# Performance work log

Hardware: AMD Instinct MI355X
Metric: run time of the kernel (lower is better)

The kernel has to match this reference:

```python
import jax, jax.numpy as jnp
import numpy as np

B, I, H, S = 16384, 256, 256, 32
EVENT_THRESH = 0.85


def setup_inputs() -> dict:
    key = jax.random.key(0)
    ks = jax.random.split(key, 20)
    r = lambda k, shp: jax.random.normal(k, shp, dtype=jnp.float32)
    w = lambda k, shp: jax.random.normal(k, shp, dtype=jnp.float32) * 0.02
    return {
        # forward args / state
        "x_t": r(ks[0], (B, I)),
        "h_lstm": r(ks[1], (B, H)),
        "c_lstm": r(ks[2], (B, H)),
        "h_mem_prev": jnp.zeros((B, H), jnp.float32),
        "slots": r(ks[3], (B, S, I)),
        "ptr": jax.random.randint(ks[4], (B,), 0, S, dtype=jnp.int64),
        # SequenceMemoryCell params (weights stored as (in, out))
        "W_val": w(ks[5], (I, I)),
        "b_val": jnp.zeros((I,), jnp.float32),
        "W_ev": w(ks[6], (I, 1)),
        "b_ev": jnp.zeros((1,), jnp.float32),
        "pos_emb": r(ks[7], (S, I)),
        "slot_weights": jnp.ones((S,), jnp.float32),
        "W_sp": w(ks[8], (I, H)),
        "b_sp": jnp.zeros((H,), jnp.float32),
        # LSTM params
        "W_ih": w(ks[9], (I + H, 4 * H)),
        "b_ih": jnp.zeros((4 * H,), jnp.float32),
        "W_hh": w(ks[10], (H, 4 * H)),
    }


def reference(x_t, h_lstm, c_lstm, h_mem_prev, slots, ptr,
              W_val, b_val, W_ev, b_ev, pos_emb, slot_weights, W_sp, b_sp,
              W_ih, b_ih, W_hh):
    n_slots = slot_weights.shape[0]
    # --- SequenceMemoryCell ---
    e_t = jax.nn.sigmoid(x_t @ W_ev + b_ev)            # (B, 1)
    v = x_t @ W_val + b_val                            # (B, I)
    event_mask = e_t[:, 0] > EVENT_THRESH              # (B,)
    # circular-buffer scatter write at ptr, gated by event_mask
    onehot = jnp.arange(n_slots)[None, :] == ptr[:, None]          # (B, S)
    write = event_mask[:, None] & onehot                           # (B, S)
    new_slots = jnp.where(write[:, :, None], v[:, None, :], slots) # (B, S, I)
    new_ptr = (ptr + event_mask.astype(ptr.dtype)) % n_slots
    # weighted pool over slots with positional embeddings
    w = jax.nn.softmax(slot_weights)                               # (S,)
    pooled = jnp.einsum('bsi,s->bi', new_slots + pos_emb[None], w) # (B, I)
    h_mem = pooled @ W_sp + b_sp                                   # (B, H)
    # --- LSTM on [x_t; h_mem] ---
    gates = jnp.concatenate([x_t, h_mem], axis=1) @ W_ih + b_ih + h_lstm @ W_hh
    i_g, f_g, g_t, o_g = jnp.split(gates, 4, axis=1)
    c_new = jax.nn.sigmoid(f_g) * c_lstm + jax.nn.sigmoid(i_g) * jnp.tanh(g_t)
    h_new = jax.nn.sigmoid(o_g) * jnp.tanh(c_new)
    return (h_new, c_new, h_mem, new_slots, new_ptr)
```

## Files before the change

### kernel.cpp

```cpp
#include <hip/hip_runtime.h>
#include <hip/hip_bf16.h>

#define B_SZ 16384
#define I_SZ 256
#define H_SZ 256
#define S_SZ 32

typedef __attribute__((ext_vector_type(8))) short short8;
typedef __attribute__((ext_vector_type(4))) float f32x4;

__device__ __forceinline__ ushort f2b(float f) {
  __hip_bfloat16 h = __float2bfloat16(f);
  return *reinterpret_cast<ushort*>(&h);
}
__device__ __forceinline__ float sgm(float x) { return 1.0f / (1.0f + expf(-x)); }

__device__ __forceinline__ void gll16(const void* g, void* l) {
  __builtin_amdgcn_global_load_lds(
      (const __attribute__((address_space(1))) unsigned*)g,
      (__attribute__((address_space(3))) unsigned*)l, 16, 0, 0);
}

__global__ __launch_bounds__(256) void front(
    const float* __restrict__ x_t, const float* __restrict__ h_lstm,
    const float* __restrict__ slots, const int* __restrict__ ptr,
    const float* __restrict__ W_val, const float* __restrict__ b_val,
    const float* __restrict__ W_ev, const float* __restrict__ b_ev,
    const float* __restrict__ pos_emb, const float* __restrict__ slot_w,
    const float* __restrict__ W_sp, const float* __restrict__ W_ih,
    const float* __restrict__ W_hh, const float* __restrict__ b_ih,
    const float* __restrict__ b_sp,
    float* __restrict__ out_slots, float* __restrict__ out_ptr,
    ushort* __restrict__ x_b, ushort* __restrict__ hl_b,
    ushort* __restrict__ pooled_b, ushort* __restrict__ WspT,
    ushort* __restrict__ WcatT, float* __restrict__ biasp) {
  __shared__ float x_sh[4][256];
  const int bid = blockIdx.x;
  const int t = threadIdx.x;

  if (bid < 4096) {
    int l = t & 63;
    int w = t >> 6;
    int b = bid * 4 + w;

    float4 x4 = *(const float4*)(x_t + (size_t)b * 256 + l * 4);
    *(float4*)&x_sh[w][l * 4] = x4;
    ushort4 xb = make_ushort4(f2b(x4.x), f2b(x4.y), f2b(x4.z), f2b(x4.w));
    *(ushort4*)&x_b[(size_t)b * 256 + l * 4] = xb;
    float4 hl4 = *(const float4*)(h_lstm + (size_t)b * 256 + l * 4);
    ushort4 hb = make_ushort4(f2b(hl4.x), f2b(hl4.y), f2b(hl4.z), f2b(hl4.w));
    *(ushort4*)&hl_b[(size_t)b * 256 + l * 4] = hb;

    float4 we4 = *(const float4*)(W_ev + l * 4);
    float p = x4.x * we4.x + x4.y * we4.y + x4.z * we4.z + x4.w * we4.w;
    for (int off = 32; off; off >>= 1) p += __shfl_xor(p, off, 64);
    float z = p + b_ev[0];
    bool ev = sgm(z) > 0.85f;
    int pb = ptr[b];

    __syncthreads();

    f32x4 v4 = {0.f, 0.f, 0.f, 0.f};
    if (ev) {
      v4 = *(const f32x4*)(b_val + l * 4);
      for (int k = 0; k < 256; k++) {
        float xv = x_sh[w][k];
        f32x4 wv = *(const f32x4*)(W_val + (size_t)k * 256 + l * 4);
        v4 += xv * wv;
      }
    }

    float mx = -1e30f;
    for (int s = 0; s < 32; s++) mx = fmaxf(mx, slot_w[s]);
    float sum = 0.f;
    for (int s = 0; s < 32; s++) sum += expf(slot_w[s] - mx);
    float rs = 1.f / sum;

    const f32x4* sl4 = (const f32x4*)slots + (size_t)b * 2048;
    f32x4* os4 = (f32x4*)out_slots + (size_t)b * 2048;
    const f32x4* pe4 = (const f32x4*)pos_emb;
    f32x4 pool = {0.f, 0.f, 0.f, 0.f};
#pragma unroll 8
    for (int s = 0; s < 32; s++) {
      float ws_ = expf(slot_w[s] - mx) * rs;
      f32x4 tv = __builtin_nontemporal_load(sl4 + s * 64 + l);
      if (ev && s == pb) tv = v4;
      __builtin_nontemporal_store(tv, os4 + s * 64 + l);
      f32x4 pe = pe4[s * 64 + l];
      pool += ws_ * (tv + pe);
    }
    ushort4 pb4 = make_ushort4(f2b(pool[0]), f2b(pool[1]), f2b(pool[2]), f2b(pool[3]));
    *(ushort4*)&pooled_b[(size_t)b * 256 + l * 4] = pb4;

    if (l == 0) out_ptr[b] = (float)(ev ? ((pb + 1) & 31) : pb);

  } else if (bid < 4104) {
    for (int e = (bid - 4096) * 256 + t; e < 65536; e += 8 * 256) {
      int n = e >> 8, k = e & 255;
      WspT[e] = f2b(W_sp[k * 256 + n]);
    }
  } else if (bid < 4168) {
    for (int e = (bid - 4104) * 256 + t; e < 1024 * 512; e += 64 * 256) {
      int r = e >> 9, kk = e & 511;
      int k = (kk < 256) ? kk : kk + 256;
      int hb = r >> 6, g = (r >> 4) & 3, hl = r & 15;
      int n = g * 256 + hb * 16 + hl;
      float v = (k < 512) ? W_ih[(size_t)k * 1024 + n]
                          : W_hh[(size_t)(k - 512) * 1024 + n];
      WcatT[(size_t)r * 768 + k] = f2b(v);
    }
  } else if (bid < 4424) {
    int i = bid - 4168;
    x_sh[0][t] = W_sp[(size_t)i * 256 + t];
    __syncthreads();
    int n0 = t * 4;
    f32x4 acc = {0.f, 0.f, 0.f, 0.f};
    for (int m = 0; m < 256; m++) {
      float s = x_sh[0][m];
      f32x4 w2 = *(const f32x4*)(W_ih + (size_t)(256 + m) * 1024 + n0);
      acc += s * w2;
    }
#pragma unroll
    for (int d = 0; d < 4; d++) {
      int n = n0 + d;
      int g = n >> 8, rem = n & 255, hb = rem >> 4, hl = rem & 15;
      int r = hb * 64 + g * 16 + hl;
      WcatT[(size_t)r * 768 + 256 + i] = f2b(acc[d]);
    }
  } else {
    int n0 = t * 4;
    f32x4 acc = *(const f32x4*)(b_ih + n0);
    for (int m = 0; m < 256; m++) {
      float s = b_sp[m];
      f32x4 w2 = *(const f32x4*)(W_ih + (size_t)(256 + m) * 1024 + n0);
      acc += s * w2;
    }
    *(f32x4*)(biasp + n0) = acc;
  }
}

__global__ __launch_bounds__(256) void gemm_hmem(
    const ushort* __restrict__ A0, const ushort* __restrict__ WT,
    const float* __restrict__ bias, float* __restrict__ out_f32) {
  int l = threadIdx.x & 63;
  int wid = threadIdx.x >> 6;
  int wm = wid >> 1, wn = wid & 1;
  int m0 = blockIdx.x * 128;
  int n0 = blockIdx.y * 128;
  __shared__ ushort Ash[128 * 32];
  __shared__ ushort Bsh[128 * 32];

  f32x4 acc[4][4] = {};

  for (int k0 = 0; k0 < 256; k0 += 32) {
#pragma unroll
    for (int i = 0; i < 2; i++) {
      int seg = i * 256 + threadIdx.x;
      int row = seg >> 2, cb = (seg & 3) * 8;
      gll16(A0 + (size_t)(m0 + row) * 256 + k0 + cb, Ash + seg * 8);
    }
#pragma unroll
    for (int i = 0; i < 2; i++) {
      int seg = i * 256 + threadIdx.x;
      int row = seg >> 2, cb = (seg & 3) * 8;
      gll16(WT + (size_t)(n0 + row) * 256 + k0 + cb, Bsh + seg * 8);
    }
    __syncthreads();

    short8 af[4], bfr[4];
#pragma unroll
    for (int m = 0; m < 4; m++)
      af[m] = *(const short8*)&Ash[(wm * 64 + m * 16 + (l & 15)) * 32 + (l >> 4) * 8];
#pragma unroll
    for (int n = 0; n < 4; n++)
      bfr[n] = *(const short8*)&Bsh[(wn * 64 + n * 16 + (l & 15)) * 32 + (l >> 4) * 8];
#pragma unroll
    for (int m = 0; m < 4; m++)
#pragma unroll
      for (int n = 0; n < 4; n++)
        acc[m][n] = __builtin_amdgcn_mfma_f32_16x16x32_bf16(af[m], bfr[n], acc[m][n], 0, 0, 0);
    __syncthreads();
  }

#pragma unroll
  for (int m = 0; m < 4; m++)
#pragma unroll
    for (int n = 0; n < 4; n++)
#pragma unroll
      for (int r = 0; r < 4; r++) {
        int row = m0 + wm * 64 + m * 16 + (l >> 4) * 4 + r;
        int col = n0 + wn * 64 + n * 16 + (l & 15);
        out_f32[(size_t)row * 256 + col] = acc[m][n][r] + bias[col];
      }
}

template <int KTOT>
__global__ __launch_bounds__(512) void gemm256_lstm(
    const ushort* __restrict__ A0s, const ushort* __restrict__ A1s,
    const ushort* __restrict__ A2s, const ushort* __restrict__ WT,
    const float* __restrict__ bias, const float* __restrict__ c_lstm,
    float* __restrict__ h_out, float* __restrict__ c_out) {
  constexpr int NT = KTOT / 64;
  __shared__ ushort Ash[2][2][128][64];
  __shared__ ushort Bsh[2][2][128][64];
  const int tid = threadIdx.x;
  const int l = tid & 63;
  const int wid = tid >> 6;
  const int wm = wid >> 2, wn = wid & 3;
  const int id = blockIdx.x;
  const int xcd = id & 7, jj = id >> 3;
  const int mb = xcd * 8 + (jj >> 2), nb = jj & 3;
  const int m0 = mb * 256, n0 = nb * 256;

  auto asel = [&](int kt) { return kt < 4 ? A0s : (kt < 8 ? A1s : A2s); };

  auto stageA = [&](int bu, int h, int kt) {
    const ushort* s = asel(kt);
    int cb = (kt & 3) * 64;
#pragma unroll
    for (int ld = 0; ld < 2; ld++) {
      int seg = ld * 512 + tid;
      int row = seg >> 3, C = seg & 7;
      int Cs = C ^ (row & 7);
      gll16(s + (size_t)(m0 + h * 128 + row) * 256 + cb + Cs * 8,
            &Ash[bu][h][0][0] + seg * 8);
    }
  };
  auto stageB = [&](int bu, int h, int kt) {
    int cb = kt * 64;
#pragma unroll
    for (int ld = 0; ld < 2; ld++) {
      int seg = ld * 512 + tid;
      int row = seg >> 3, C = seg & 7;
      int Cs = C ^ (row & 7);
      gll16(WT + (size_t)(n0 + h * 128 + row) * KTOT + cb + Cs * 8,
            &Bsh[bu][h][0][0] + seg * 8);
    }
  };

  f32x4 acc[8][4] = {};

  stageB(0, 0, 0); stageB(0, 1, 0);
  stageA(0, 0, 0); stageA(0, 1, 0);
  stageB(1, 0, 1); stageB(1, 1, 1);

  for (int t = 0; t < NT; t++) {
    const int c = t & 1;
    const ushort* Abase = &Ash[c][wm][0][0];
    const ushort* Bbase = &Bsh[c][wn >> 1][0][0];

    if (t < NT - 1) asm volatile("s_waitcnt vmcnt(4)" ::: "memory");
    else            asm volatile("s_waitcnt vmcnt(0)" ::: "memory");
    asm volatile("s_barrier" ::: "memory");

    short8 bfr[4][2];
#pragma unroll
    for (int nf = 0; nf < 4; nf++)
#pragma unroll
      for (int kk = 0; kk < 2; kk++) {
        int r = (wn & 1) * 64 + nf * 16 + (l & 15);
        int C = (kk * 4 + (l >> 4)) ^ (l & 7);
        bfr[nf][kk] = *(const short8*)(Bbase + r * 64 + C * 8);
      }
    short8 af[2][2];
#pragma unroll
    for (int q = 0; q < 2; q++)
#pragma unroll
      for (int kk = 0; kk < 2; kk++) {
        int r = (0 * 2 + q) * 16 + (l & 15);
        int C = (kk * 4 + (l >> 4)) ^ (l & 7);
        af[q][kk] = *(const short8*)(Abase + r * 64 + C * 8);
      }
    if (t + 1 < NT) stageA(c ^ 1, 0, t + 1);
    __builtin_amdgcn_s_setprio(1);
#pragma unroll
    for (int q = 0; q < 2; q++)
#pragma unroll
      for (int nf = 0; nf < 4; nf++)
#pragma unroll
        for (int kk = 0; kk < 2; kk++)
          acc[q][nf] = __builtin_amdgcn_mfma_f32_16x16x32_bf16(
              af[q][kk], bfr[nf][kk], acc[q][nf], 0, 0, 0);
    __builtin_amdgcn_s_setprio(0);

#pragma unroll
    for (int p = 1; p < 4; p++) {
      asm volatile("s_barrier" ::: "memory");
#pragma unroll
      for (int q = 0; q < 2; q++)
#pragma unroll
        for (int kk = 0; kk < 2; kk++) {
          int r = (p * 2 + q) * 16 + (l & 15);
          int C = (kk * 4 + (l >> 4)) ^ (l & 7);
          af[q][kk] = *(const short8*)(Abase + r * 64 + C * 8);
        }
      if (p == 1) {
        if (t + 1 < NT) stageA(c ^ 1, 1, t + 1);
        if (t + 2 < NT) stageB(c, 0, t + 2);
      } else if (p == 2) {
        if (t + 2 < NT) stageB(c, 1, t + 2);
      }
      __builtin_amdgcn_s_setprio(1);
#pragma unroll
      for (int q = 0; q < 2; q++)
#pragma unroll
        for (int nf = 0; nf < 4; nf++)
#pragma unroll
          for (int kk = 0; kk < 2; kk++)
            acc[p * 2 + q][nf] = __builtin_amdgcn_mfma_f32_16x16x32_bf16(
                af[q][kk], bfr[nf][kk], acc[p * 2 + q][nf], 0, 0, 0);
      __builtin_amdgcn_s_setprio(0);
    }
  }

  int h = (nb * 4 + wn) * 16 + (l & 15);
  float bi = bias[h], bf_ = bias[256 + h], bg = bias[512 + h], bo = bias[768 + h];
#pragma unroll
  for (int mf = 0; mf < 8; mf++)
#pragma unroll
    for (int r = 0; r < 4; r++) {
      int row = m0 + wm * 128 + mf * 16 + (l >> 4) * 4 + r;
      float ig = acc[mf][0][r] + bi;
      float fg = acc[mf][1][r] + bf_;
      float gt = acc[mf][2][r] + bg;
      float og = acc[mf][3][r] + bo;
      float cc = c_lstm[(size_t)row * 256 + h];
      float cn = sgm(fg) * cc + sgm(ig) * tanhf(gt);
      float hn = sgm(og) * tanhf(cn);
      c_out[(size_t)row * 256 + h] = cn;
      h_out[(size_t)row * 256 + h] = hn;
    }
}

extern "C" void kernel_launch(void* const* d_in, const int* in_sizes, int n_in,
                              void* d_out, int out_size, void* d_ws, size_t ws_size,
                              hipStream_t stream) {
  const float* x_t    = (const float*)d_in[0];
  const float* h_lstm = (const float*)d_in[1];
  const float* c_lstm = (const float*)d_in[2];
  const float* slots  = (const float*)d_in[4];
  const int*   ptr    = (const int*)d_in[5];
  const float* W_val  = (const float*)d_in[6];
  const float* b_val  = (const float*)d_in[7];
  const float* W_ev   = (const float*)d_in[8];
  const float* b_ev   = (const float*)d_in[9];
  const float* pos_emb = (const float*)d_in[10];
  const float* slot_w  = (const float*)d_in[11];
  const float* W_sp   = (const float*)d_in[12];
  const float* b_sp   = (const float*)d_in[13];
  const float* W_ih   = (const float*)d_in[14];
  const float* b_ih   = (const float*)d_in[15];
  const float* W_hh   = (const float*)d_in[16];

  float* out = (float*)d_out;
  const size_t BH = (size_t)B_SZ * H_SZ;
  float* out_h    = out;
  float* out_c    = out + BH;
  float* out_hmem = out + 2 * BH;
  float* out_slots = out + 3 * BH;
  float* out_ptr   = out + 3 * BH + (size_t)B_SZ * S_SZ * I_SZ;

  char* ws = (char*)d_ws;
  ushort* x_b      = (ushort*)(ws);
  ushort* hl_b     = (ushort*)(ws + 8388608);
  ushort* pooled_b = (ushort*)(ws + 16777216);
  ushort* WspT     = (ushort*)(ws + 25165824);
  ushort* WcatT    = (ushort*)(ws + 25296896);
  float*  biasp    = (float*)(ws + 26869760);

  front<<<4425, 256, 0, stream>>>(
      x_t, h_lstm, slots, ptr, W_val, b_val, W_ev, b_ev, pos_emb, slot_w,
      W_sp, W_ih, W_hh, b_ih, b_sp,
      out_slots, out_ptr, x_b, hl_b, pooled_b, WspT, WcatT, biasp);

  gemm256_lstm<768><<<256, 512, 0, stream>>>(
      x_b, pooled_b, hl_b, WcatT, biasp, c_lstm, out_h, out_c);

  gemm_hmem<<<dim3(128, 2), 256, 0, stream>>>(
      pooled_b, WspT, b_sp, out_hmem);
}
```

Baseline: 251.4 us.

## Fold h_mem GEMM into LSTM GEMM launch and precompute softmax weights in LDS

Removes the separate gemm_hmem kernel and adds 64 extra blocks to the LSTM GEMM launch. Each of these blocks computes a 256x256 tile of pooled@W_sp with the same pipelined 256-tile loop, using 4 K-steps instead of 12. This saves a launch and its tail, and puts the small h_mem GEMM on CUs left idle by the 256-block main grid. Separately, the front kernel computes the slot softmax once per block with wave shuffles and stores it in shared memory, instead of every thread looping over slot_w with exp. The trade-off is a runtime tile count (nt) and block-type branches inside the GEMM kernel, which may cost some unrolling or register efficiency.

Measured after the change: 253.1 us. No clear change (+0.7%).

```diff
diff --git a/kernel.cpp b/kernel.cpp
--- a/kernel.cpp
+++ b/kernel.cpp
@@ -35,6 +35,7 @@
     ushort* __restrict__ pooled_b, ushort* __restrict__ WspT,
     ushort* __restrict__ WcatT, float* __restrict__ biasp) {
   __shared__ float x_sh[4][256];
+  __shared__ float w_sh[32];
   const int bid = blockIdx.x;
   const int t = threadIdx.x;
 
@@ -42,6 +43,18 @@
     int l = t & 63;
     int w = t >> 6;
     int b = bid * 4 + w;
+
+    if (t < 32) {
+      float v = slot_w[t];
+      float m = v;
+#pragma unroll
+      for (int off = 16; off; off >>= 1) m = fmaxf(m, __shfl_xor(m, off));
+      float e = expf(v - m);
+      float s2 = e;
+#pragma unroll
+      for (int off = 16; off; off >>= 1) s2 += __shfl_xor(s2, off);
+      w_sh[t] = e / s2;
+    }
 
     float4 x4 = *(const float4*)(x_t + (size_t)b * 256 + l * 4);
     *(float4*)&x_sh[w][l * 4] = x4;
@@ -70,19 +83,13 @@
       }
     }
 
-    float mx = -1e30f;
-    for (int s = 0; s < 32; s++) mx = fmaxf(mx, slot_w[s]);
-    float sum = 0.f;
-    for (int s = 0; s < 32; s++) sum += expf(slot_w[s] - mx);
-    float rs = 1.f / sum;
-
     const f32x4* sl4 = (const f32x4*)slots + (size_t)b * 2048;
     f32x4* os4 = (f32x4*)out_slots + (size_t)b * 2048;
     const f32x4* pe4 = (const f32x4*)pos_emb;
     f32x4 pool = {0.f, 0.f, 0.f, 0.f};
 #pragma unroll 8
     for (int s = 0; s < 32; s++) {
-      float ws_ = expf(slot_w[s] - mx) * rs;
+      float ws_ = w_sh[s];
       f32x4 tv = __builtin_nontemporal_load(sl4 + s * 64 + l);
       if (ev && s == pb) tv = v4;
       __builtin_nontemporal_store(tv, os4 + s * 64 + l);
@@ -139,68 +146,14 @@
   }
 }
 
-__global__ __launch_bounds__(256) void gemm_hmem(
-    const ushort* __restrict__ A0, const ushort* __restrict__ WT,
-    const float* __restrict__ bias, float* __restrict__ out_f32) {
-  int l = threadIdx.x & 63;
-  int wid = threadIdx.x >> 6;
-  int wm = wid >> 1, wn = wid & 1;
-  int m0 = blockIdx.x * 128;
-  int n0 = blockIdx.y * 128;
-  __shared__ ushort Ash[128 * 32];
-  __shared__ ushort Bsh[128 * 32];
-
-  f32x4 acc[4][4] = {};
-
-  for (int k0 = 0; k0 < 256; k0 += 32) {
-#pragma unroll
-    for (int i = 0; i < 2; i++) {
-      int seg = i * 256 + threadIdx.x;
-      int row = seg >> 2, cb = (seg & 3) * 8;
-      gll16(A0 + (size_t)(m0 + row) * 256 + k0 + cb, Ash + seg * 8);
-    }
-#pragma unroll
-    for (int i = 0; i < 2; i++) {
-      int seg = i * 256 + threadIdx.x;
-      int row = seg >> 2, cb = (seg & 3) * 8;
-      gll16(WT + (size_t)(n0 + row) * 256 + k0 + cb, Bsh + seg * 8);
-    }
-    __syncthreads();
-
-    short8 af[4], bfr[4];
-#pragma unroll
-    for (int m = 0; m < 4; m++)
-      af[m] = *(const short8*)&Ash[(wm * 64 + m * 16 + (l & 15)) * 32 + (l >> 4) * 8];
-#pragma unroll
-    for (int n = 0; n < 4; n++)
-      bfr[n] = *(const short8*)&Bsh[(wn * 64 + n * 16 + (l & 15)) * 32 + (l >> 4) * 8];
-#pragma unroll
-    for (int m = 0; m < 4; m++)
-#pragma unroll
-      for (int n = 0; n < 4; n++)
-        acc[m][n] = __builtin_amdgcn_mfma_f32_16x16x32_bf16(af[m], bfr[n], acc[m][n], 0, 0, 0);
-    __syncthreads();
-  }
-
-#pragma unroll
-  for (int m = 0; m < 4; m++)
-#pragma unroll
-    for (int n = 0; n < 4; n++)
-#pragma unroll
-      for (int r = 0; r < 4; r++) {
-        int row = m0 + wm * 64 + m * 16 + (l >> 4) * 4 + r;
-        int col = n0 + wn * 64 + n * 16 + (l & 15);
-        out_f32[(size_t)row * 256 + col] = acc[m][n][r] + bias[col];
-      }
-}
-
 template <int KTOT>
-__global__ __launch_bounds__(512) void gemm256_lstm(
+__global__ __launch_bounds__(512) void gemm256_fused(
     const ushort* __restrict__ A0s, const ushort* __restrict__ A1s,
     const ushort* __restrict__ A2s, const ushort* __restrict__ WT,
-    const float* __restrict__ bias, const float* __restrict__ c_lstm,
-    float* __restrict__ h_out, float* __restrict__ c_out) {
-  constexpr int NT = KTOT / 64;
+    const ushort* __restrict__ WspT, const float* __restrict__ bias,
+    const float* __restrict__ b_sp, const float* __restrict__ c_lstm,
+    float* __restrict__ h_out, float* __restrict__ c_out,
+    float* __restrict__ hmem_out) {
   __shared__ ushort Ash[2][2][128][64];
   __shared__ ushort Bsh[2][2][128][64];
   const int tid = threadIdx.x;
@@ -208,11 +161,23 @@
   const int wid = tid >> 6;
   const int wm = wid >> 2, wn = wid & 3;
   const int id = blockIdx.x;
-  const int xcd = id & 7, jj = id >> 3;
-  const int mb = xcd * 8 + (jj >> 2), nb = jj & 3;
-  const int m0 = mb * 256, n0 = nb * 256;
-
-  auto asel = [&](int kt) { return kt < 4 ? A0s : (kt < 8 ? A1s : A2s); };
+  const bool hm = id >= 256;
+  int m0, n0, nb = 0;
+  if (!hm) {
+    const int xcd = id & 7, jj = id >> 3;
+    const int mb = xcd * 8 + (jj >> 2);
+    nb = jj & 3;
+    m0 = mb * 256; n0 = nb * 256;
+  } else {
+    m0 = (id - 256) * 256; n0 = 0;
+  }
+  const int nt = hm ? 4 : 12;
+  const ushort* Bp = hm ? WspT : WT;
+  const int Bstride = hm ? 256 : KTOT;
+
+  auto asel = [&](int kt) {
+    return hm ? A1s : (kt < 4 ? A0s : (kt < 8 ? A1s : A2s));
+  };
 
   auto stageA = [&](int bu, int h, int kt) {
     const ushort* s = asel(kt);
@@ -233,7 +198,7 @@
       int seg = ld * 512 + tid;
       int row = seg >> 3, C = seg & 7;
       int Cs = C ^ (row & 7);
-      gll16(WT + (size_t)(n0 + h * 128 + row) * KTOT + cb + Cs * 8,
+      gll16(Bp + (size_t)(n0 + h * 128 + row) * Bstride + cb + Cs * 8,
             &Bsh[bu][h][0][0] + seg * 8);
     }
   };
@@ -244,12 +209,12 @@
   stageA(0, 0, 0); stageA(0, 1, 0);
   stageB(1, 0, 1); stageB(1, 1, 1);
 
-  for (int t = 0; t < NT; t++) {
+  for (int t = 0; t < nt; t++) {
     const int c = t & 1;
     const ushort* Abase = &Ash[c][wm][0][0];
     const ushort* Bbase = &Bsh[c][wn >> 1][0][0];
 
-    if (t < NT - 1) asm volatile("s_waitcnt vmcnt(4)" ::: "memory");
+    if (t < nt - 1) asm volatile("s_waitcnt vmcnt(4)" ::: "memory");
     else            asm volatile("s_waitcnt vmcnt(0)" ::: "memory");
     asm volatile("s_barrier" ::: "memory");
 
@@ -271,7 +236,7 @@
         int C = (kk * 4 + (l >> 4)) ^ (l & 7);
         af[q][kk] = *(const short8*)(Abase + r * 64 + C * 8);
       }
-    if (t + 1 < NT) stageA(c ^ 1, 0, t + 1);
+    if (t + 1 < nt) stageA(c ^ 1, 0, t + 1);
     __builtin_amdgcn_s_setprio(1);
 #pragma unroll
     for (int q = 0; q < 2; q++)
@@ -295,10 +260,10 @@
           af[q][kk] = *(const short8*)(Abase + r * 64 + C * 8);
         }
       if (p == 1) {
-        if (t + 1 < NT) stageA(c ^ 1, 1, t + 1);
-        if (t + 2 < NT) stageB(c, 0, t + 2);
+        if (t + 1 < nt) stageA(c ^ 1, 1, t + 1);
+        if (t + 2 < nt) stageB(c, 0, t + 2);
       } else if (p == 2) {
-        if (t + 2 < NT) stageB(c, 1, t + 2);
+        if (t + 2 < nt) stageB(c, 1, t + 2);
       }
       __builtin_amdgcn_s_setprio(1);
 #pragma unroll
@@ -313,23 +278,38 @@
     }
   }
 
-  int h = (nb * 4 + wn) * 16 + (l & 15);
-  float bi = bias[h], bf_ = bias[256 + h], bg = bias[512 + h], bo = bias[768 + h];
-#pragma unroll
-  for (int mf = 0; mf < 8; mf++)
-#pragma unroll
-    for (int r = 0; r < 4; r++) {
-      int row = m0 + wm * 128 + mf * 16 + (l >> 4) * 4 + r;
-      float ig = acc[mf][0][r] + bi;
-      float fg = acc[mf][1][r] + bf_;
-      float gt = acc[mf][2][r] + bg;
-      float og = acc[mf][3][r] + bo;
-      float cc = c_lstm[(size_t)row * 256 + h];
-      float cn = sgm(fg) * cc + sgm(ig) * tanhf(gt);
-      float hn = sgm(og) * tanhf(cn);
-      c_out[(size_t)row * 256 + h] = cn;
-      h_out[(size_t)row * 256 + h] = hn;
-    }
+  if (!hm) {
+    int h = (nb * 4 + wn) * 16 + (l & 15);
+    float bi = bias[h], bf_ = bias[256 + h], bg = bias[512 + h], bo = bias[768 + h];
+#pragma unroll
+    for (int mf = 0; mf < 8; mf++)
+#pragma unroll
+      for (int r = 0; r < 4; r++) {
+        int row = m0 + wm * 128 + mf * 16 + (l >> 4) * 4 + r;
+        float ig = acc[mf][0][r] + bi;
+        float fg = acc[mf][1][r] + bf_;
+        float gt = acc[mf][2][r] + bg;
+        float og = acc[mf][3][r] + bo;
+        float cc = c_lstm[(size_t)row * 256 + h];
+        float cn = sgm(fg) * cc + sgm(ig) * tanhf(gt);
+        float hn = sgm(og) * tanhf(cn);
+        c_out[(size_t)row * 256 + h] = cn;
+        h_out[(size_t)row * 256 + h] = hn;
+      }
+  } else {
+#pragma unroll
+    for (int nf = 0; nf < 4; nf++) {
+      int col = wn * 64 + nf * 16 + (l & 15);
+      float bb = b_sp[col];
+#pragma unroll
+      for (int mf = 0; mf < 8; mf++)
+#pragma unroll
+        for (int r = 0; r < 4; r++) {
+          int row = m0 + wm * 128 + mf * 16 + (l >> 4) * 4 + r;
+          hmem_out[(size_t)row * 256 + col] = acc[mf][nf][r] + bb;
+        }
+    }
+  }
 }
 
 extern "C" void kernel_launch(void* const* d_in, const int* in_sizes, int n_in,
@@ -373,9 +353,7 @@
       W_sp, W_ih, W_hh, b_ih, b_sp,
       out_slots, out_ptr, x_b, hl_b, pooled_b, WspT, WcatT, biasp);
 
-  gemm256_lstm<768><<<256, 512, 0, stream>>>(
-      x_b, pooled_b, hl_b, WcatT, biasp, c_lstm, out_h, out_c);
-
-  gemm_hmem<<<dim3(128, 2), 256, 0, stream>>>(
-      pooled_b, WspT, b_sp, out_hmem);
-}
+  gemm256_fused<768><<<320, 512, 0, stream>>>(
+      x_b, pooled_b, hl_b, WcatT, WspT, biasp, b_sp, c_lstm,
+      out_h, out_c, out_hmem);
+}
```
